# Performance work log

Hardware: AMD Instinct MI355X
Metric: run time of the kernel (lower is better)

Reference implementation:

```python
import jax, jax.numpy as jnp
import numpy as np

N = 10000
E = 160000
NT = 4      # num_types
NB = 8      # bessel basis size
U = 32      # env_embed_multiplicity
R_MAX = 6.0
AVG_NEIGH = 16.0
POLY_P = 6.0


def _mlp(x, Ws):
    # nequip ScalarMLPFunction: no biases, forward-normalized weights, SiLU between layers
    n = len(Ws)
    for i, W in enumerate(Ws):
        x = x @ (W * (1.0 / jnp.sqrt(jnp.float32(W.shape[0]))))
        if i < n - 1:
            x = jax.nn.silu(x)
    return x


def _poly_cutoff(r, rc, p=POLY_P):
    x = r / rc
    out = (1.0 - ((p + 1.0) * (p + 2.0) / 2.0) * x ** p
           + p * (p + 2.0) * x ** (p + 1.0)
           - (p * (p + 1.0) / 2.0) * x ** (p + 2.0))
    return out * (x < 1.0)


def _weighted_channels(edge_attr, w):
    # MakeWeightedChannels: per-edge, per-channel weight for each irrep block
    # edge_attr: [E,4] = (0e | 1o), w: [E,U,2] -> out [E,U,4]
    wd = jnp.concatenate([w[:, :, 0:1], jnp.repeat(w[:, :, 1:2], 3, axis=-1)], axis=-1)
    return edge_attr[:, None, :] * wd


def _forward(edge_index, node_attrs, edge_attr, edge_embed, edge_length,
             W2b0, W2b1, W2b2, Wenv0, Wlat0, Wlat1, Wenv1, Wfin0, Wfin1,
             Wlin_s, Wlin_v, resnet_params):
    n_nodes = node_attrs.shape[0]
    n_edges = edge_attr.shape[0]
    center, neigh = edge_index[0], edge_index[1]
    cut = _poly_cutoff(edge_length, R_MAX)[:, None]           # [E,1], same per-layer cutoff
    env_norm = 1.0 / jnp.sqrt(AVG_NEIGH)
    sqrt3 = jnp.sqrt(3.0)
    c = jnp.exp(resnet_params)                                 # resnet update coefficients

    # ---- two-body latent (layer 0 latent)
    lat_in = jnp.concatenate([node_attrs[center], node_attrs[neigh], edge_embed], axis=-1)
    latents = _mlp(lat_in, [W2b0, W2b1, W2b2]) * cut           # [E,512]
    norm2 = c[0] ** 2
    latents = latents * (c[0] / jnp.sqrt(norm2))

    # env-embed MLP layer 0: feature weights + env weights
    w0 = _mlp(latents, [Wenv0])                                # [E,4U]
    w_feat = w0[:, :2 * U].reshape(n_edges, U, 2)
    w_env = w0[:, 2 * U:].reshape(n_edges, U, 2)
    features = _weighted_channels(edge_attr, w_feat)           # [E,U,4]

    def env_embed_edges(w_env):
        env_w = _weighted_channels(edge_attr, w_env)           # [E,U,4]
        env = jax.ops.segment_sum(env_w, center, num_segments=n_nodes) * env_norm
        return env[center]                                     # [E,U,4]

    # ---- layer 0 TP ('uuu', e3nn component norm): (0e+1o) x (0e+1o) -> [0e,0e,1o,1o]
    env_e = env_embed_edges(w_env)
    t0 = features[:, :, 0] * env_e[:, :, 0]
    t1 = jnp.sum(features[:, :, 1:] * env_e[:, :, 1:], axis=-1) / sqrt3
    v0 = features[:, :, 0:1] * env_e[:, :, 1:]
    v1 = features[:, :, 1:] * env_e[:, :, 0:1]
    scalars = jnp.concatenate([t0, t1], axis=-1)               # [E,2U]
    # e3nn Linear mixing full_out_irreps back to (0e+1o) x U
    alpha = 1.0 / jnp.sqrt(2.0 * U)
    y_s = (scalars @ Wlin_s) * alpha                           # [E,U]
    x_v = jnp.concatenate([v0, v1], axis=1)                    # [E,2U,3]
    y_v = jnp.einsum('ekd,ko->eod', x_v, Wlin_v) * alpha       # [E,U,3]
    features = jnp.concatenate([y_s[..., None], y_v], axis=-1)

    # latent resnet update
    new_lat = _mlp(jnp.concatenate([latents, scalars], axis=-1), [Wlat0, Wlat1]) * cut
    latents = (jnp.sqrt(norm2) * latents + c[1] * new_lat) / jnp.sqrt(norm2 + c[1] ** 2)
    norm2 = norm2 + c[1] ** 2

    w_env = _mlp(latents, [Wenv1]).reshape(n_edges, U, 2)

    # ---- layer 1 TP (last layer): only scalar outputs [0e,0e]
    env_e = env_embed_edges(w_env)
    t0 = features[:, :, 0] * env_e[:, :, 0]
    t1 = jnp.sum(features[:, :, 1:] * env_e[:, :, 1:], axis=-1) / sqrt3
    scalars = jnp.concatenate([t0, t1], axis=-1)               # [E,2U]
    # (the last-layer Linear output features are never used downstream -> skipped)

    # ---- final latent
    new_lat = _mlp(jnp.concatenate([latents, scalars], axis=-1), [Wfin0, Wfin1]) * cut
    latents = (jnp.sqrt(norm2) * latents + c[2] * new_lat) / jnp.sqrt(norm2 + c[2] ** 2)
    return latents                                             # [E,512] edge features


def setup_inputs() -> dict:
    key = jax.random.key(0)
    ks = jax.random.split(key, 20)
    edge_index = jax.random.randint(ks[0], (2, E), 0, N)
    node_types = jax.random.randint(ks[1], (N,), 0, NT)
    node_attrs = jax.nn.one_hot(node_types, NT, dtype=jnp.float32)
    edge_length = jax.random.uniform(ks[2], (E,), minval=0.5, maxval=R_MAX)
    vec = jax.random.normal(ks[3], (E, 3), dtype=jnp.float32)
    unit = vec / jnp.linalg.norm(vec, axis=-1, keepdims=True)
    # component-normalized real spherical harmonics: l=0 -> 1, l=1 -> sqrt(3)*unit
    edge_attr = jnp.concatenate([jnp.ones((E, 1), jnp.float32), jnp.sqrt(3.0) * unit], axis=-1)
    nb = jnp.arange(1, NB + 1, dtype=jnp.float32)
    edge_embed = (jnp.sqrt(2.0 / R_MAX)
                  * jnp.sin(nb[None, :] * jnp.pi * edge_length[:, None] / R_MAX)
                  / edge_length[:, None])
    w = lambda k, shp: jax.random.normal(k, shp, dtype=jnp.float32)
    return {
        'edge_index': edge_index, 'node_attrs': node_attrs, 'edge_attr': edge_attr,
        'edge_embed': edge_embed, 'edge_length': edge_length,
        'W2b0': w(ks[4], (2 * NT + NB, 128)), 'W2b1': w(ks[5], (128, 256)), 'W2b2': w(ks[6], (256, 512)),
        'Wenv0': w(ks[7], (512, 4 * U)),
        'Wlat0': w(ks[8], (512 + 2 * U, 512)), 'Wlat1': w(ks[9], (512, 512)),
        'Wenv1': w(ks[10], (512, 2 * U)),
        'Wfin0': w(ks[11], (512 + 2 * U, 512)), 'Wfin1': w(ks[12], (512, 512)),
        'Wlin_s': w(ks[13], (2 * U, U)), 'Wlin_v': w(ks[14], (2 * U, U)),
        'resnet_params': jnp.zeros((3,), jnp.float32),
    }


def reference(edge_index, node_attrs, edge_attr, edge_embed, edge_length,
              W2b0, W2b1, W2b2, Wenv0, Wlat0, Wlat1, Wenv1, Wfin0, Wfin1,
              Wlin_s, Wlin_v, resnet_params):
    return _forward(edge_index, node_attrs, edge_attr, edge_embed, edge_length,
                    W2b0, W2b1, W2b2, Wenv0, Wlat0, Wlat1, Wenv1, Wfin0, Wfin1,
                    Wlin_s, Wlin_v, resnet_params)
```

## Files before the change

kernel.cpp:

```cpp
#include <hip/hip_runtime.h>
#include <math.h>

#define E_EDGES 160000
#define N_NODES 10000

typedef __attribute__((ext_vector_type(8))) __bf16 bf16x8;
typedef __attribute__((ext_vector_type(4))) float f32x4;
typedef __attribute__((ext_vector_type(4))) unsigned int u32x4;

__device__ __forceinline__ unsigned short f2bf(float x) {
    unsigned u = __float_as_uint(x);
    u += 0x7fff + ((u >> 16) & 1);
    return (unsigned short)(u >> 16);
}
__device__ __forceinline__ float bf2f(unsigned short h) {
    return __uint_as_float(((unsigned)h) << 16);
}
__device__ __forceinline__ void gload16(const unsigned short* g, unsigned short* l) {
    __builtin_amdgcn_global_load_lds(
        (const __attribute__((address_space(1))) void*)g,
        (__attribute__((address_space(3))) void*)l, 16, 0, 0);
}

__global__ __launch_bounds__(256)
void prep_kernel(const int* __restrict__ ei, const float* __restrict__ na,
                 const float* __restrict__ embed, const float* __restrict__ elen,
                 float* __restrict__ cut, unsigned short* __restrict__ A16b,
                 int* __restrict__ deg)
{
    int e = blockIdx.x * blockDim.x + threadIdx.x;
    if (e >= E_EDGES) return;
    float r  = elen[e];
    float x  = r * (1.0f / 6.0f);
    float x2 = x * x;
    float x6 = x2 * x2 * x2;
    float c = 1.0f - 28.0f * x6 + 48.0f * x6 * x - 21.0f * x6 * x2;
    cut[e] = (x < 1.0f) ? c : 0.0f;
    int ctr = ei[e];
    int ngh = ei[E_EDGES + e];
    atomicAdd(&deg[ctr], 1);
    float4 ac = *(const float4*)(na + (size_t)ctr * 4);
    float4 an = *(const float4*)(na + (size_t)ngh * 4);
    float4 b0 = *(const float4*)(embed + (size_t)e * 8);
    float4 b1 = *(const float4*)(embed + (size_t)e * 8 + 4);
    unsigned short* o = A16b + (size_t)e * 32;
    o[0]  = f2bf(ac.x); o[1]  = f2bf(ac.y); o[2]  = f2bf(ac.z); o[3]  = f2bf(ac.w);
    o[4]  = f2bf(an.x); o[5]  = f2bf(an.y); o[6]  = f2bf(an.z); o[7]  = f2bf(an.w);
    o[8]  = f2bf(b0.x); o[9]  = f2bf(b0.y); o[10] = f2bf(b0.z); o[11] = f2bf(b0.w);
    o[12] = f2bf(b1.x); o[13] = f2bf(b1.y); o[14] = f2bf(b1.z); o[15] = f2bf(b1.w);
    #pragma unroll
    for (int i = 16; i < 32; ++i) o[i] = 0;
}

__global__ __launch_bounds__(256)
void wtrans_all(const float* __restrict__ w0, const float* __restrict__ w1,
                const float* __restrict__ w2, const float* __restrict__ w3,
                const float* __restrict__ w4, const float* __restrict__ w5,
                const float* __restrict__ w6, const float* __restrict__ w7,
                const float* __restrict__ w8, unsigned short* __restrict__ wbuf)
{
    int blk = blockIdx.x;
    const float* W; int K, N, Kpad, Npad; size_t dbase; int lstart; float sc;
    const float s16  = 0.25f;
    const float s128 = 0.088388347648318447f;
    const float s256 = 0.0625f;
    const float s512 = 0.044194173824159223f;
    const float s576 = 0.041666666666666664f;
    if      (blk <   16) { W=w0; K=16;  N=128; Kpad=32;  Npad=128; dbase=0;       lstart=0;    sc=s16;  }
    else if (blk <  144) { W=w1; K=128; N=256; Kpad=128; Npad=256; dbase=4096;    lstart=16;   sc=s128; }
    else if (blk <  656) { W=w2; K=256; N=512; Kpad=256; Npad=512; dbase=36864;   lstart=144;  sc=s256; }
    else if (blk <  912) { W=w3; K=512; N=128; Kpad=512; Npad=128; dbase=167936;  lstart=656;  sc=s512; }
    else if (blk < 2064) { W=w4; K=576; N=512; Kpad=576; Npad=512; dbase=233472;  lstart=912;  sc=s576; }
    else if (blk < 3088) { W=w5; K=512; N=512; Kpad=512; Npad=512; dbase=528384;  lstart=2064; sc=s512; }
    else if (blk < 3344) { W=w6; K=512; N=64;  Kpad=512; Npad=128; dbase=790528;  lstart=3088; sc=s512; }
    else if (blk < 4496) { W=w7; K=576; N=512; Kpad=576; Npad=512; dbase=856064;  lstart=3344; sc=s576; }
    else                 { W=w8; K=512; N=512; Kpad=512; Npad=512; dbase=1150976; lstart=4496; sc=s512; }
    int local = (blk - lstart) * 256 + threadIdx.x;
    int n = local % Npad, k = local / Npad;
    if (k >= Kpad) return;
    float v = (k < K && n < N) ? W[(size_t)k * N + n] * sc : 0.0f;
    wbuf[dbase + (size_t)n * Kpad + k] = f2bf(v);
}

__global__ __launch_bounds__(1024)
void scan_kernel(const int* __restrict__ deg, int* __restrict__ offs)
{
    __shared__ int part[1024];
    int t = threadIdx.x;
    int base = t * 10;
    int loc[10];
    int s = 0;
    #pragma unroll
    for (int i = 0; i < 10; ++i) {
        int idx = base + i;
        int d = (idx < N_NODES) ? deg[idx] : 0;
        loc[i] = s; s += d;
    }
    part[t] = s;
    __syncthreads();
    for (int o = 1; o < 1024; o <<= 1) {
        int v = (t >= o) ? part[t - o] : 0;
        __syncthreads();
        part[t] += v;
        __syncthreads();
    }
    int excl = (t > 0) ? part[t - 1] : 0;
    #pragma unroll
    for (int i = 0; i < 10; ++i) {
        int idx = base + i;
        if (idx < N_NODES) offs[idx] = excl + loc[i];
    }
    if (t == 1023) offs[N_NODES] = part[1023];
}

__global__ __launch_bounds__(256)
void fill_kernel(const int* __restrict__ ei, const int* __restrict__ offs,
                 int* __restrict__ cnt, int* __restrict__ elist)
{
    int e = blockIdx.x * blockDim.x + threadIdx.x;
    if (e >= E_EDGES) return;
    int c = ei[e];
    int pos = offs[c] + atomicAdd(&cnt[c], 1);
    elist[pos] = e;
}

__global__ __launch_bounds__(256)
void sortseg_kernel(const int* __restrict__ offs, int* __restrict__ elist)
{
    int node = blockIdx.x * 4 + (threadIdx.x >> 6);
    int l = threadIdx.x & 63;
    if (node >= N_NODES) return;
    int b = offs[node], en = offs[node + 1];
    int deg = en - b;
    if (deg <= 1) return;
    if (deg <= 64) {
        int v = (l < deg) ? elist[b + l] : 0x7fffffff;
        #pragma unroll
        for (int k = 2; k <= 64; k <<= 1) {
            #pragma unroll
            for (int j = k >> 1; j > 0; j >>= 1) {
                int o = __shfl_xor(v, j);
                bool dirUp = ((l & k) == 0);
                bool lower = ((l & j) == 0);
                int mn = v < o ? v : o;
                int mx = v < o ? o : v;
                v = (dirUp == lower) ? mn : mx;
            }
        }
        if (l < deg) elist[b + l] = v;
    } else if (l == 0) {
        for (int i = b + 1; i < en; ++i) {
            int v = elist[i];
            int j = i - 1;
            while (j >= b && elist[j] > v) { elist[j + 1] = elist[j]; --j; }
            elist[j + 1] = v;
        }
    }
}

__global__ __launch_bounds__(256)
void envgather_kernel(const unsigned short* __restrict__ Wb, int wstride, int woff,
                      const float* __restrict__ ea, const int* __restrict__ offs,
                      const int* __restrict__ elist, float* __restrict__ env)
{
    int n = blockIdx.x * 2 + (threadIdx.x >> 7);
    int t = threadIdx.x & 127;
    if (n >= N_NODES) return;
    int u = t >> 2, comp = t & 3;
    int widx = woff + u * 2 + (comp ? 1 : 0);
    int beg = offs[n], end = offs[n + 1];
    float acc = 0.0f;
    for (int i = beg; i < end; ++i) {
        int e = elist[i];
        float w = bf2f(Wb[(size_t)e * wstride + widx]);
        float a = ea[(size_t)e * 4 + comp];
        acc += a * w;
    }
    env[(size_t)n * 128 + t] = acc * 0.25f;
}

template<int EPIL, bool CONCAT>
__global__ __launch_bounds__(256)
void gemm_bf16(const unsigned short* __restrict__ A1, const unsigned short* __restrict__ A2,
               int KA1, int K, const unsigned short* __restrict__ Bt,
               int nx, int ldc, int Nstore,
               float* __restrict__ Cf, unsigned short* __restrict__ Cb,
               const float* __restrict__ cut, const float* __restrict__ rp)
{
    __shared__ __align__(16) unsigned short SB[3][2][128 * 32];
    const int tid  = threadIdx.x;
    const int lane = tid & 63;
    const int wid  = tid >> 6;
    const int wr   = wid >> 1, wc = wid & 1;
    const int nwg = gridDim.x;
    const int fid = blockIdx.x;
    const int q = nwg >> 3, r = nwg & 7;
    const int xcd = fid & 7, j = fid >> 3;
    const int L = ((xcd < r) ? xcd * (q + 1) : r * (q + 1) + (xcd - r) * q) + j;
    const int bn = (L % nx) * 128;
    const int bm = (L / nx) * 128;

    const int l15 = lane & 15;
    const int l4r = lane >> 2;
    const int sk8 = (((lane & 3) ^ ((lane >> 3) & 3)) << 3);
    const int rk8 = ((((lane >> 4) ^ ((l15 >> 1) & 3)) & 3) << 3);
    const int KA2 = K - KA1;
    const int T   = K >> 5;

    f32x4 acc[4][4] = {};

    auto stage = [&](int t, int b) {
        int k0 = t << 5;
        #pragma unroll
        for (int i = 0; i < 2; ++i) {
            int ch  = (wid << 1) + i;
            int row = (ch << 4) + l4r;
            const unsigned short* gp;
            if (!CONCAT || k0 < KA1)
                gp = A1 + (size_t)(bm + row) * KA1 + k0 + sk8;
            else
                gp = A2 + (size_t)(bm + row) * KA2 + (k0 - KA1) + sk8;
            gload16(gp, &SB[b][0][ch << 9]);
            const unsigned short* gpb = Bt + (size_t)(bn + row) * K + k0 + sk8;
            gload16(gpb, &SB[b][1][ch << 9]);
        }
    };

    stage(0, 0);
    if (T >= 2) stage(1, 1);

    for (int t = 0; t < T; ++t) {
        if (t < T - 1) asm volatile("s_waitcnt vmcnt(4)" ::: "memory");
        else           asm volatile("s_waitcnt vmcnt(0)" ::: "memory");
        __builtin_amdgcn_s_barrier();
        __builtin_amdgcn_sched_barrier(0);

        if (t + 2 < T) stage(t + 2, (t + 2) % 3);

        const unsigned short* As = &SB[t % 3][0][0];
        const unsigned short* Bs = &SB[t % 3][1][0];
        bf16x8 af[4], bfr[4];
        #pragma unroll
        for (int m = 0; m < 4; ++m)
            af[m] = __builtin_bit_cast(bf16x8, *(const u32x4*)&As[(wr * 64 + m * 16 + l15) * 32 + rk8]);
        #pragma unroll
        for (int n = 0; n < 4; ++n)
            bfr[n] = __builtin_bit_cast(bf16x8, *(const u32x4*)&Bs[(wc * 64 + n * 16 + l15) * 32 + rk8]);

        __builtin_amdgcn_s_setprio(1);
        #pragma unroll
        for (int m = 0; m < 4; ++m)
            #pragma unroll
            for (int n = 0; n < 4; ++n)
                acc[m][n] = __builtin_amdgcn_mfma_f32_16x16x32_bf16(af[m], bfr[n], acc[m][n], 0, 0, 0);
        __builtin_amdgcn_s_setprio(0);

        asm volatile("s_waitcnt lgkmcnt(0)" ::: "memory");
        __builtin_amdgcn_sched_barrier(0);
    }

    float c0 = 1.0f, c1 = 1.0f, c2 = 1.0f;
    if (EPIL >= 3) { c0 = __expf(rp[0]); c1 = __expf(rp[1]); c2 = __expf(rp[2]); }

    #pragma unroll
    for (int m = 0; m < 4; ++m) {
        int rbase = bm + wr * 64 + m * 16 + ((lane >> 4) << 2);
        #pragma unroll
        for (int n = 0; n < 4; ++n) {
            int col = bn + wc * 64 + n * 16 + l15;
            if (col < Nstore) {
                #pragma unroll
                for (int rr = 0; rr < 4; ++rr) {
                    int row = rbase + rr;
                    float v = acc[m][n][rr];
                    size_t off2 = (size_t)row * ldc + col;
                    if (EPIL == 0) {
                        Cb[off2] = f2bf(v);
                    } else if (EPIL == 1) {
                        v = v / (1.0f + __expf(-v));
                        Cb[off2] = f2bf(v);
                    } else if (EPIL == 2) {
                        v *= cut[row];
                        Cb[off2] = f2bf(v);
                    } else if (EPIL == 3) {
                        float old = bf2f(Cb[off2]);
                        v = (c0 * old + c1 * v * cut[row]) * rsqrtf(c0 * c0 + c1 * c1);
                        Cb[off2] = f2bf(v);
                    } else {
                        float old = bf2f(Cb[off2]);
                        float n2 = c0 * c0 + c1 * c1;
                        v = (sqrtf(n2) * old + c2 * v * cut[row]) * rsqrtf(n2 + c2 * c2);
                        Cf[off2] = v;
                    }
                }
            }
        }
    }
}

__global__ __launch_bounds__(256)
void tp0_kernel(const unsigned short* __restrict__ W0b, const float* __restrict__ ea,
                const float* __restrict__ env, const int* __restrict__ ei,
                const float* __restrict__ Ws, const float* __restrict__ Wv,
                unsigned short* __restrict__ scalb, unsigned short* __restrict__ feat2b)
{
    __shared__ float sc[8][64];
    __shared__ float xv[8][64][3];
    __shared__ float Wsl[2048];
    __shared__ float Wvl[2048];
    int tid = threadIdx.x;
    const float alpha = 0.125f;
    #pragma unroll
    for (int i = 0; i < 8; ++i) {
        Wsl[tid + i * 256] = Ws[tid + i * 256] * alpha;
        Wvl[tid + i * 256] = Wv[tid + i * 256] * alpha;
    }
    int le = tid >> 5;
    int u  = tid & 31;
    int e  = blockIdx.x * 8 + le;
    int c  = ei[e];
    float4 a = *(const float4*)(ea + (size_t)e * 4);
    const float* ep = env + (size_t)c * 128 + u * 4;
    float e0 = ep[0], e1 = ep[1], e2 = ep[2], e3 = ep[3];
    float wf0 = bf2f(W0b[(size_t)e * 128 + u * 2]);
    float wf1 = bf2f(W0b[(size_t)e * 128 + u * 2 + 1]);
    float f0 = a.x * wf0;
    float f1 = a.y * wf1, f2 = a.z * wf1, f3 = a.w * wf1;
    const float rs3 = 0.57735026918962576f;
    float t0 = f0 * e0;
    float t1 = (f1 * e1 + f2 * e2 + f3 * e3) * rs3;
    scalb[(size_t)e * 64 + u]      = f2bf(t0);
    scalb[(size_t)e * 64 + 32 + u] = f2bf(t1);
    sc[le][u]      = t0;
    sc[le][32 + u] = t1;
    xv[le][u][0] = f0 * e1; xv[le][u][1] = f0 * e2; xv[le][u][2] = f0 * e3;
    xv[le][32 + u][0] = f1 * e0; xv[le][32 + u][1] = f2 * e0; xv[le][32 + u][2] = f3 * e0;
    __syncthreads();
    float ys = 0.0f, yv0 = 0.0f, yv1 = 0.0f, yv2 = 0.0f;
    #pragma unroll 8
    for (int k = 0; k < 64; ++k) {
        float ws = Wsl[k * 32 + u];
        float wv = Wvl[k * 32 + u];
        ys  = fmaf(sc[le][k], ws, ys);
        yv0 = fmaf(xv[le][k][0], wv, yv0);
        yv1 = fmaf(xv[le][k][1], wv, yv1);
        yv2 = fmaf(xv[le][k][2], wv, yv2);
    }
    ushort4 ov;
    ov.x = f2bf(ys);
    ov.y = f2bf(yv0);
    ov.z = f2bf(yv1);
    ov.w = f2bf(yv2);
    *(ushort4*)(feat2b + (size_t)e * 128 + u * 4) = ov;
}

__global__ __launch_bounds__(256)
void tp1_kernel(const unsigned short* __restrict__ feat2b, const float* __restrict__ env,
                const int* __restrict__ ei, unsigned short* __restrict__ scalb)
{
    int idx = blockIdx.x * blockDim.x + threadIdx.x;
    if (idx >= E_EDGES * 32) return;
    int e = idx >> 5, u = idx & 31;
    int c = ei[e];
    const float* ep = env + (size_t)c * 128 + u * 4;
    ushort4 f4 = *(const ushort4*)(feat2b + (size_t)e * 128 + u * 4);
    float fx = bf2f(f4.x), fy = bf2f(f4.y), fz = bf2f(f4.z), fw = bf2f(f4.w);
    const float rs3 = 0.57735026918962576f;
    float t0 = fx * ep[0];
    float t1 = (fy * ep[1] + fz * ep[2] + fw * ep[3]) * rs3;
    scalb[(size_t)e * 64 + u]      = f2bf(t0);
    scalb[(size_t)e * 64 + 32 + u] = f2bf(t1);
}

extern "C" void kernel_launch(void* const* d_in, const int* in_sizes, int n_in,
                              void* d_out, int out_size, void* d_ws, size_t ws_size,
                              hipStream_t stream)
{
    const int*   ei     = (const int*)d_in[0];
    const float* na     = (const float*)d_in[1];
    const float* ea     = (const float*)d_in[2];
    const float* embed  = (const float*)d_in[3];
    const float* elen   = (const float*)d_in[4];
    const float* W2b0   = (const float*)d_in[5];
    const float* W2b1   = (const float*)d_in[6];
    const float* W2b2   = (const float*)d_in[7];
    const float* Wenv0  = (const float*)d_in[8];
    const float* Wlat0  = (const float*)d_in[9];
    const float* Wlat1  = (const float*)d_in[10];
    const float* Wenv1  = (const float*)d_in[11];
    const float* Wfin0  = (const float*)d_in[12];
    const float* Wfin1  = (const float*)d_in[13];
    const float* Wlin_s = (const float*)d_in[14];
    const float* Wlin_v = (const float*)d_in[15];
    const float* rp     = (const float*)d_in[16];

    float* L = (float*)d_out;
    const size_t E = E_EDGES;

    char* ws = (char*)d_ws;
    size_t off = 0;
    auto alloc = [&](size_t b) { void* p = ws + off; off += (b + 255) & ~(size_t)255; return p; };
    float*          cutb   = (float*)alloc(E * 4);
    unsigned short* wbuf   = (unsigned short*)alloc((size_t)1413120 * 2);
    float*          envb   = (float*)alloc((size_t)N_NODES * 128 * 4);
    unsigned short* scalb  = (unsigned short*)alloc(E * 64 * 2);
    unsigned short* feat2b = (unsigned short*)alloc(E * 128 * 2);
    unsigned short* Lb     = (unsigned short*)alloc(E * 512 * 2);
    int*            degcnt = (int*)alloc((size_t)2 * N_NODES * 4);
    int*            offs   = (int*)alloc((N_NODES + 1) * 4);
    int*            elist  = (int*)alloc(E * 4);
    unsigned short* A16b   = (unsigned short*)alloc(E * 32 * 2);
    unsigned short* H1b    = (unsigned short*)alloc(E * 128 * 2);
    unsigned short* H2b    = (unsigned short*)alloc(E * 256 * 2);
    unsigned short* R1b    = (unsigned short*)alloc(E * 128 * 2);
    unsigned short* NLb    = (unsigned short*)alloc(E * 512 * 2);
    unsigned short* WE1b   = (unsigned short*)alloc(E * 64 * 2);
    int* deg = degcnt;
    int* cnt = degcnt + N_NODES;

    unsigned short* W2b0t  = wbuf;
    unsigned short* W2b1t  = wbuf + 4096;
    unsigned short* W2b2t  = wbuf + 36864;
    unsigned short* Wenv0t = wbuf + 167936;
    unsigned short* Wlat0t = wbuf + 233472;
    unsigned short* Wlat1t = wbuf + 528384;
    unsigned short* Wenv1t = wbuf + 790528;
    unsigned short* Wfin0t = wbuf + 856064;
    unsigned short* Wfin1t = wbuf + 1150976;
    wtrans_all<<<5520, 256, 0, stream>>>(W2b0, W2b1, W2b2, Wenv0, Wlat0, Wlat1,
                                         Wenv1, Wfin0, Wfin1, wbuf);

    hipMemsetAsync(degcnt, 0, (size_t)2 * N_NODES * 4, stream);
    prep_kernel<<<E_EDGES / 256, 256, 0, stream>>>(ei, na, embed, elen, cutb, A16b, deg);
    scan_kernel<<<1, 1024, 0, stream>>>(deg, offs);
    fill_kernel<<<E_EDGES / 256, 256, 0, stream>>>(ei, offs, cnt, elist);
    sortseg_kernel<<<N_NODES / 4, 256, 0, stream>>>(offs, elist);

    gemm_bf16<1, false><<<1250, 256, 0, stream>>>(A16b, nullptr, 32, 32, W2b0t, 1, 128, 128, nullptr, H1b, nullptr, nullptr);
    gemm_bf16<1, false><<<2500, 256, 0, stream>>>(H1b, nullptr, 128, 128, W2b1t, 2, 256, 256, nullptr, H2b, nullptr, nullptr);
    gemm_bf16<2, false><<<5000, 256, 0, stream>>>(H2b, nullptr, 256, 256, W2b2t, 4, 512, 512, nullptr, Lb, cutb, nullptr);

    gemm_bf16<0, false><<<1250, 256, 0, stream>>>(Lb, nullptr, 512, 512, Wenv0t, 1, 128, 128, nullptr, R1b, nullptr, nullptr);

    envgather_kernel<<<N_NODES / 2, 256, 0, stream>>>(R1b, 128, 64, ea, offs, elist, envb);
    tp0_kernel<<<E_EDGES / 8, 256, 0, stream>>>(R1b, ea, envb, ei, Wlin_s, Wlin_v, scalb, feat2b);

    gemm_bf16<1, true ><<<5000, 256, 0, stream>>>(Lb, scalb, 512, 576, Wlat0t, 4, 512, 512, nullptr, NLb, nullptr, nullptr);
    gemm_bf16<3, false><<<5000, 256, 0, stream>>>(NLb, nullptr, 512, 512, Wlat1t, 4, 512, 512, nullptr, Lb, cutb, rp);

    gemm_bf16<0, false><<<1250, 256, 0, stream>>>(Lb, nullptr, 512, 512, Wenv1t, 1, 64, 64, nullptr, WE1b, nullptr, nullptr);

    envgather_kernel<<<N_NODES / 2, 256, 0, stream>>>(WE1b, 64, 0, ea, offs, elist, envb);
    tp1_kernel<<<E_EDGES * 32 / 256, 256, 0, stream>>>(feat2b, envb, ei, scalb);

    gemm_bf16<1, true ><<<5000, 256, 0, stream>>>(Lb, scalb, 512, 576, Wfin0t, 4, 512, 512, nullptr, NLb, nullptr, nullptr);
    gemm_bf16<4, false><<<5000, 256, 0, stream>>>(NLb, nullptr, 512, 512, Wfin1t, 4, 512, 512, L, Lb, cutb, rp);
}
```

Before: 1.325 ms.

## Enlarge bf16 GEMM tiles to 256x128 with 8-wave workgroups

The bf16 MFMA GEMM now has each workgroup compute a 256x128 output tile with 512 threads instead of 128x128 with 256 threads. A-tile staging doubles while B is staged once per wave, so each loaded weight tile is reused across twice as many rows and the vmcnt wait is adjusted to match. Intermediate buffers are padded and a row guard (M_STORE) limits stores, but launching 626 row tiles means stores still reach past the real edge count. It is unclear whether the fp32 output path stays within bounds for those extra rows.

```diff
diff --git a/kernel.cpp b/kernel.cpp
--- a/kernel.cpp
+++ b/kernel.cpp
@@ -3,6 +3,7 @@
 
 #define E_EDGES 160000
 #define N_NODES 10000
+#define M_STORE 160128
 
 typedef __attribute__((ext_vector_type(8))) __bf16 bf16x8;
 typedef __attribute__((ext_vector_type(4))) float f32x4;
@@ -180,25 +181,27 @@
 }
 
 template<int EPIL, bool CONCAT>
-__global__ __launch_bounds__(256)
+__global__ __launch_bounds__(512)
 void gemm_bf16(const unsigned short* __restrict__ A1, const unsigned short* __restrict__ A2,
                int KA1, int K, const unsigned short* __restrict__ Bt,
                int nx, int ldc, int Nstore,
                float* __restrict__ Cf, unsigned short* __restrict__ Cb,
                const float* __restrict__ cut, const float* __restrict__ rp)
 {
-    __shared__ __align__(16) unsigned short SB[3][2][128 * 32];
+    __shared__ __align__(16) unsigned short SBA[3][256 * 32];
+    __shared__ __align__(16) unsigned short SBB[3][128 * 32];
     const int tid  = threadIdx.x;
     const int lane = tid & 63;
     const int wid  = tid >> 6;
-    const int wr   = wid >> 1, wc = wid & 1;
+    const int wr   = wid >> 1;
+    const int wc   = wid & 1;
     const int nwg = gridDim.x;
     const int fid = blockIdx.x;
     const int q = nwg >> 3, r = nwg & 7;
-    const int xcd = fid & 7, j = fid >> 3;
-    const int L = ((xcd < r) ? xcd * (q + 1) : r * (q + 1) + (xcd - r) * q) + j;
+    const int xcd = fid & 7, jj = fid >> 3;
+    const int L = ((xcd < r) ? xcd * (q + 1) : r * (q + 1) + (xcd - r) * q) + jj;
     const int bn = (L % nx) * 128;
-    const int bm = (L / nx) * 128;
+    const int bm = (L / nx) * 256;
 
     const int l15 = lane & 15;
     const int l4r = lane >> 2;
@@ -220,25 +223,25 @@
                 gp = A1 + (size_t)(bm + row) * KA1 + k0 + sk8;
             else
                 gp = A2 + (size_t)(bm + row) * KA2 + (k0 - KA1) + sk8;
-            gload16(gp, &SB[b][0][ch << 9]);
-            const unsigned short* gpb = Bt + (size_t)(bn + row) * K + k0 + sk8;
-            gload16(gpb, &SB[b][1][ch << 9]);
+            gload16(gp, &SBA[b][ch << 9]);
         }
+        int rowb = (wid << 4) + l4r;
+        gload16(Bt + (size_t)(bn + rowb) * K + k0 + sk8, &SBB[b][wid << 9]);
     };
 
     stage(0, 0);
     if (T >= 2) stage(1, 1);
 
     for (int t = 0; t < T; ++t) {
-        if (t < T - 1) asm volatile("s_waitcnt vmcnt(4)" ::: "memory");
+        if (t < T - 1) asm volatile("s_waitcnt vmcnt(3)" ::: "memory");
         else           asm volatile("s_waitcnt vmcnt(0)" ::: "memory");
         __builtin_amdgcn_s_barrier();
         __builtin_amdgcn_sched_barrier(0);
 
         if (t + 2 < T) stage(t + 2, (t + 2) % 3);
 
-        const unsigned short* As = &SB[t % 3][0][0];
-        const unsigned short* Bs = &SB[t % 3][1][0];
+        const unsigned short* As = &SBA[t % 3][0];
+        const unsigned short* Bs = &SBB[t % 3][0];
         bf16x8 af[4], bfr[4];
         #pragma unroll
         for (int m = 0; m < 4; ++m)
@@ -272,6 +275,7 @@
                 #pragma unroll
                 for (int rr = 0; rr < 4; ++rr) {
                     int row = rbase + rr;
+                    if (row >= M_STORE) continue;
                     float v = acc[m][n][rr];
                     size_t off2 = (size_t)row * ldc + col;
                     if (EPIL == 0) {
@@ -395,26 +399,27 @@
     const float* rp     = (const float*)d_in[16];
 
     float* L = (float*)d_out;
-    const size_t E = E_EDGES;
+    const size_t E  = E_EDGES;
+    const size_t EP = M_STORE + 128;
 
     char* ws = (char*)d_ws;
     size_t off = 0;
     auto alloc = [&](size_t b) { void* p = ws + off; off += (b + 255) & ~(size_t)255; return p; };
-    float*          cutb   = (float*)alloc(E * 4);
+    float*          cutb   = (float*)alloc(EP * 4);
     unsigned short* wbuf   = (unsigned short*)alloc((size_t)1413120 * 2);
     float*          envb   = (float*)alloc((size_t)N_NODES * 128 * 4);
-    unsigned short* scalb  = (unsigned short*)alloc(E * 64 * 2);
+    unsigned short* scalb  = (unsigned short*)alloc(EP * 64 * 2);
     unsigned short* feat2b = (unsigned short*)alloc(E * 128 * 2);
-    unsigned short* Lb     = (unsigned short*)alloc(E * 512 * 2);
+    unsigned short* Lb     = (unsigned short*)alloc(EP * 512 * 2);
     int*            degcnt = (int*)alloc((size_t)2 * N_NODES * 4);
     int*            offs   = (int*)alloc((N_NODES + 1) * 4);
     int*            elist  = (int*)alloc(E * 4);
-    unsigned short* A16b   = (unsigned short*)alloc(E * 32 * 2);
-    unsigned short* H1b    = (unsigned short*)alloc(E * 128 * 2);
-    unsigned short* H2b    = (unsigned short*)alloc(E * 256 * 2);
-    unsigned short* R1b    = (unsigned short*)alloc(E * 128 * 2);
-    unsigned short* NLb    = (unsigned short*)alloc(E * 512 * 2);
-    unsigned short* WE1b   = (unsigned short*)alloc(E * 64 * 2);
+    unsigned short* A16b   = (unsigned short*)alloc(EP * 32 * 2);
+    unsigned short* H1b    = (unsigned short*)alloc(EP * 128 * 2);
+    unsigned short* H2b    = (unsigned short*)alloc(EP * 256 * 2);
+    unsigned short* R1b    = (unsigned short*)alloc(EP * 128 * 2);
+    unsigned short* NLb    = (unsigned short*)alloc(EP * 512 * 2);
+    unsigned short* WE1b   = (unsigned short*)alloc(EP * 64 * 2);
     int* deg = degcnt;
     int* cnt = degcnt + N_NODES;
 
@@ -436,23 +441,25 @@
     fill_kernel<<<E_EDGES / 256, 256, 0, stream>>>(ei, offs, cnt, elist);
     sortseg_kernel<<<N_NODES / 4, 256, 0, stream>>>(offs, elist);
 
-    gemm_bf16<1, false><<<1250, 256, 0, stream>>>(A16b, nullptr, 32, 32, W2b0t, 1, 128, 128, nullptr, H1b, nullptr, nullptr);
-    gemm_bf16<1, false><<<2500, 256, 0, stream>>>(H1b, nullptr, 128, 128, W2b1t, 2, 256, 256, nullptr, H2b, nullptr, nullptr);
-    gemm_bf16<2, false><<<5000, 256, 0, stream>>>(H2b, nullptr, 256, 256, W2b2t, 4, 512, 512, nullptr, Lb, cutb, nullptr);
-
-    gemm_bf16<0, false><<<1250, 256, 0, stream>>>(Lb, nullptr, 512, 512, Wenv0t, 1, 128, 128, nullptr, R1b, nullptr, nullptr);
+    const int NY = 626;
+
+    gemm_bf16<1, false><<<NY * 1, 512, 0, stream>>>(A16b, nullptr, 32, 32, W2b0t, 1, 128, 128, nullptr, H1b, nullptr, nullptr);
+    gemm_bf16<1, false><<<NY * 2, 512, 0, stream>>>(H1b, nullptr, 128, 128, W2b1t, 2, 256, 256, nullptr, H2b, nullptr, nullptr);
+    gemm_bf16<2, false><<<NY * 4, 512, 0, stream>>>(H2b, nullptr, 256, 256, W2b2t, 4, 512, 512, nullptr, Lb, cutb, nullptr);
+
+    gemm_bf16<0, false><<<NY * 1, 512, 0, stream>>>(Lb, nullptr, 512, 512, Wenv0t, 1, 128, 128, nullptr, R1b, nullptr, nullptr);
 
     envgather_kernel<<<N_NODES / 2, 256, 0, stream>>>(R1b, 128, 64, ea, offs, elist, envb);
     tp0_kernel<<<E_EDGES / 8, 256, 0, stream>>>(R1b, ea, envb, ei, Wlin_s, Wlin_v, scalb, feat2b);
 
-    gemm_bf16<1, true ><<<5000, 256, 0, stream>>>(Lb, scalb, 512, 576, Wlat0t, 4, 512, 512, nullptr, NLb, nullptr, nullptr);
-    gemm_bf16<3, false><<<5000, 256, 0, stream>>>(NLb, nullptr, 512, 512, Wlat1t, 4, 512, 512, nullptr, Lb, cutb, rp);
-
-    gemm_bf16<0, false><<<1250, 256, 0, stream>>>(Lb, nullptr, 512, 512, Wenv1t, 1, 64, 64, nullptr, WE1b, nullptr, nullptr);
+    gemm_bf16<1, true ><<<NY * 4, 512, 0, stream>>>(Lb, scalb, 512, 576, Wlat0t, 4, 512, 512, nullptr, NLb, nullptr, nullptr);
+    gemm_bf16<3, false><<<NY * 4, 512, 0, stream>>>(NLb, nullptr, 512, 512, Wlat1t, 4, 512, 512, nullptr, Lb, cutb, rp);
+
+    gemm_bf16<0, false><<<NY * 1, 512, 0, stream>>>(Lb, nullptr, 512, 512, Wenv1t, 1, 64, 64, nullptr, WE1b, nullptr, nullptr);
 
     envgather_kernel<<<N_NODES / 2, 256, 0, stream>>>(WE1b, 64, 0, ea, offs, elist, envb);
     tp1_kernel<<<E_EDGES * 32 / 256, 256, 0, stream>>>(feat2b, envb, ei, scalb);
 
-    gemm_bf16<1, true ><<<5000, 256, 0, stream>>>(Lb, scalb, 512, 576, Wfin0t, 4, 512, 512, nullptr, NLb, nullptr, nullptr);
-    gemm_bf16<4, false><<<5000, 256, 0, stream>>>(NLb, nullptr, 512, 512, Wfin1t, 4, 512, 512, L, Lb, cutb, rp);
-}
+    gemm_bf16<1, true ><<<NY * 4, 512, 0, stream>>>(Lb, scalb, 512, 576, Wfin0t, 4, 512, 512, nullptr, NLb, nullptr, nullptr);
+    gemm_bf16<4, false><<<NY * 4, 512, 0, stream>>>(NLb, nullptr, 512, 512, Wfin1t, 4, 512, 512, L, Lb, cutb, rp);
+}
```

Result: slower. 1.435 ms (+8.3%).

## Fuse two-layer latent MLPs into one kernel keeping hidden activations in LDS

Applied to the files above, without the earlier changes.

Replaces each pair of GEMM launches (576->512 with SiLU, then 512->512 with the resnet update) by a single kernel. A 128-row tile's hidden layer is held in a swizzled 128KB LDS buffer, which removes the write and re-read of the E x 512 intermediate buffer through global memory. Weight fragments are loaded straight from global memory instead of being staged in LDS. The large LDS footprint limits occupancy to one block per CU, and there is no double buffering in the second GEMM loop.

```diff
diff --git a/kernel.cpp b/kernel.cpp
--- a/kernel.cpp
+++ b/kernel.cpp
@@ -259,9 +259,6 @@
         __builtin_amdgcn_sched_barrier(0);
     }
 
-    float c0 = 1.0f, c1 = 1.0f, c2 = 1.0f;
-    if (EPIL >= 3) { c0 = __expf(rp[0]); c1 = __expf(rp[1]); c2 = __expf(rp[2]); }
-
     #pragma unroll
     for (int m = 0; m < 4; ++m) {
         int rbase = bm + wr * 64 + m * 16 + ((lane >> 4) << 2);
@@ -282,16 +279,144 @@
                     } else if (EPIL == 2) {
                         v *= cut[row];
                         Cb[off2] = f2bf(v);
-                    } else if (EPIL == 3) {
-                        float old = bf2f(Cb[off2]);
-                        v = (c0 * old + c1 * v * cut[row]) * rsqrtf(c0 * c0 + c1 * c1);
-                        Cb[off2] = f2bf(v);
-                    } else {
-                        float old = bf2f(Cb[off2]);
-                        float n2 = c0 * c0 + c1 * c1;
-                        v = (sqrtf(n2) * old + c2 * v * cut[row]) * rsqrtf(n2 + c2 * c2);
-                        Cf[off2] = v;
                     }
+                }
+            }
+        }
+    }
+}
+
+template<int EPIL2>
+__global__ __launch_bounds__(512)
+void fused_mlp(const unsigned short* __restrict__ A1,
+               const unsigned short* __restrict__ A2,
+               const unsigned short* __restrict__ W1t,
+               const unsigned short* __restrict__ W2t,
+               float* __restrict__ Cf, unsigned short* __restrict__ Cb,
+               const float* __restrict__ cut, const float* __restrict__ rp)
+{
+    __shared__ __align__(16) unsigned short Hl[128 * 512];
+    __shared__ __align__(16) unsigned short SA[3][128 * 32];
+    const int tid  = threadIdx.x;
+    const int lane = tid & 63;
+    const int wid  = tid >> 6;
+    const int l15  = lane & 15;
+    const int l4r  = lane >> 2;
+    const int lk8  = (lane >> 4) << 3;
+    const int sk8  = (((lane & 3) ^ ((lane >> 3) & 3)) << 3);
+    const int rk8  = ((((lane >> 4) ^ ((l15 >> 1) & 3)) & 3) << 3);
+    const int bm   = blockIdx.x * 128;
+    const int hcol0 = wid * 64;
+    const int ocol0 = wid * 64;
+
+    auto stage = [&](int t, int b) {
+        int k0 = t << 5;
+        int row = (wid << 4) + l4r;
+        const unsigned short* gp;
+        if (k0 < 512) gp = A1 + (size_t)(bm + row) * 512 + k0 + sk8;
+        else          gp = A2 + (size_t)(bm + row) * 64 + (k0 - 512) + sk8;
+        gload16(gp, &SA[b][wid << 9]);
+    };
+
+    f32x4 acc1[8][4] = {};
+    stage(0, 0);
+    stage(1, 1);
+
+    for (int t = 0; t < 18; ++t) {
+        __builtin_amdgcn_sched_barrier(0);
+        if (t < 17) asm volatile("s_waitcnt vmcnt(1)" ::: "memory");
+        else        asm volatile("s_waitcnt vmcnt(0)" ::: "memory");
+        __builtin_amdgcn_s_barrier();
+        __builtin_amdgcn_sched_barrier(0);
+
+        const unsigned short* As = &SA[t % 3][0];
+        int k0 = t << 5;
+        bf16x8 af[8], wf[4];
+        #pragma unroll
+        for (int mi = 0; mi < 8; ++mi)
+            af[mi] = __builtin_bit_cast(bf16x8, *(const u32x4*)&As[(mi * 16 + l15) * 32 + rk8]);
+        #pragma unroll
+        for (int ni = 0; ni < 4; ++ni) {
+            int hc = hcol0 + ni * 16 + l15;
+            wf[ni] = __builtin_bit_cast(bf16x8, *(const u32x4*)(W1t + (size_t)hc * 576 + k0 + lk8));
+        }
+        __builtin_amdgcn_sched_barrier(0);
+        if (t + 2 < 18) stage(t + 2, (t + 2) % 3);
+        __builtin_amdgcn_sched_barrier(0);
+        asm volatile("s_waitcnt lgkmcnt(0)" ::: "memory");
+        __builtin_amdgcn_sched_barrier(0);
+
+        __builtin_amdgcn_s_setprio(1);
+        #pragma unroll
+        for (int mi = 0; mi < 8; ++mi)
+            #pragma unroll
+            for (int ni = 0; ni < 4; ++ni)
+                acc1[mi][ni] = __builtin_amdgcn_mfma_f32_16x16x32_bf16(af[mi], wf[ni], acc1[mi][ni], 0, 0, 0);
+        __builtin_amdgcn_s_setprio(0);
+    }
+
+    #pragma unroll
+    for (int mi = 0; mi < 8; ++mi)
+        #pragma unroll
+        for (int ni = 0; ni < 4; ++ni)
+            #pragma unroll
+            for (int rr = 0; rr < 4; ++rr) {
+                int er = mi * 16 + ((lane >> 4) << 2) + rr;
+                int hc = hcol0 + ni * 16 + l15;
+                float v = acc1[mi][ni][rr];
+                v = v / (1.0f + __expf(-v));
+                int slotp = (hc >> 3) ^ (er & 7);
+                Hl[er * 512 + slotp * 8 + (hc & 7)] = f2bf(v);
+            }
+    asm volatile("s_waitcnt lgkmcnt(0)" ::: "memory");
+    __builtin_amdgcn_s_barrier();
+    __builtin_amdgcn_sched_barrier(0);
+
+    f32x4 acc2[8][4] = {};
+    #pragma unroll 1
+    for (int kt = 0; kt < 16; ++kt) {
+        bf16x8 hf[8], w2f[4];
+        #pragma unroll
+        for (int fa = 0; fa < 8; ++fa) {
+            int er = fa * 16 + l15;
+            int slotp = (kt * 4 + (lane >> 4)) ^ (er & 7);
+            hf[fa] = __builtin_bit_cast(bf16x8, *(const u32x4*)&Hl[er * 512 + slotp * 8]);
+        }
+        #pragma unroll
+        for (int fb = 0; fb < 4; ++fb) {
+            int oc = ocol0 + fb * 16 + l15;
+            w2f[fb] = __builtin_bit_cast(bf16x8, *(const u32x4*)(W2t + (size_t)oc * 512 + kt * 32 + lk8));
+        }
+        __builtin_amdgcn_s_setprio(1);
+        #pragma unroll
+        for (int fa = 0; fa < 8; ++fa)
+            #pragma unroll
+            for (int fb = 0; fb < 4; ++fb)
+                acc2[fa][fb] = __builtin_amdgcn_mfma_f32_16x16x32_bf16(hf[fa], w2f[fb], acc2[fa][fb], 0, 0, 0);
+        __builtin_amdgcn_s_setprio(0);
+    }
+
+    float c0 = __expf(rp[0]), c1 = __expf(rp[1]), c2 = __expf(rp[2]);
+    #pragma unroll
+    for (int fa = 0; fa < 8; ++fa) {
+        int rbase = bm + fa * 16 + ((lane >> 4) << 2);
+        #pragma unroll
+        for (int fb = 0; fb < 4; ++fb) {
+            int col = ocol0 + fb * 16 + l15;
+            #pragma unroll
+            for (int rr = 0; rr < 4; ++rr) {
+                int row = rbase + rr;
+                float v = acc2[fa][fb][rr];
+                size_t off2 = (size_t)row * 512 + col;
+                if (EPIL2 == 3) {
+                    float old = bf2f(Cb[off2]);
+                    v = (c0 * old + c1 * v * cut[row]) * rsqrtf(c0 * c0 + c1 * c1);
+                    Cb[off2] = f2bf(v);
+                } else {
+                    float old = bf2f(Cb[off2]);
+                    float n2 = c0 * c0 + c1 * c1;
+                    v = (sqrtf(n2) * old + c2 * v * cut[row]) * rsqrtf(n2 + c2 * c2);
+                    Cf[off2] = v;
                 }
             }
         }
@@ -413,7 +538,6 @@
     unsigned short* H1b    = (unsigned short*)alloc(E * 128 * 2);
     unsigned short* H2b    = (unsigned short*)alloc(E * 256 * 2);
     unsigned short* R1b    = (unsigned short*)alloc(E * 128 * 2);
-    unsigned short* NLb    = (unsigned short*)alloc(E * 512 * 2);
     unsigned short* WE1b   = (unsigned short*)alloc(E * 64 * 2);
     int* deg = degcnt;
     int* cnt = degcnt + N_NODES;
@@ -445,14 +569,12 @@
     envgather_kernel<<<N_NODES / 2, 256, 0, stream>>>(R1b, 128, 64, ea, offs, elist, envb);
     tp0_kernel<<<E_EDGES / 8, 256, 0, stream>>>(R1b, ea, envb, ei, Wlin_s, Wlin_v, scalb, feat2b);
 
-    gemm_bf16<1, true ><<<5000, 256, 0, stream>>>(Lb, scalb, 512, 576, Wlat0t, 4, 512, 512, nullptr, NLb, nullptr, nullptr);
-    gemm_bf16<3, false><<<5000, 256, 0, stream>>>(NLb, nullptr, 512, 512, Wlat1t, 4, 512, 512, nullptr, Lb, cutb, rp);
+    fused_mlp<3><<<1250, 512, 0, stream>>>(Lb, scalb, Wlat0t, Wlat1t, nullptr, Lb, cutb, rp);
 
     gemm_bf16<0, false><<<1250, 256, 0, stream>>>(Lb, nullptr, 512, 512, Wenv1t, 1, 64, 64, nullptr, WE1b, nullptr, nullptr);
 
     envgather_kernel<<<N_NODES / 2, 256, 0, stream>>>(WE1b, 64, 0, ea, offs, elist, envb);
     tp1_kernel<<<E_EDGES * 32 / 256, 256, 0, stream>>>(feat2b, envb, ei, scalb);
 
-    gemm_bf16<1, true ><<<5000, 256, 0, stream>>>(Lb, scalb, 512, 576, Wfin0t, 4, 512, 512, nullptr, NLb, nullptr, nullptr);
-    gemm_bf16<4, false><<<5000, 256, 0, stream>>>(NLb, nullptr, 512, 512, Wfin1t, 4, 512, 512, L, Lb, cutb, rp);
-}
+    fused_mlp<4><<<1250, 512, 0, stream>>>(Lb, scalb, Wfin0t, Wfin1t, L, Lb, cutb, rp);
+}
```

New measurement: 1.183 ms. -10.7%, faster.
